# Optimization experiments

Measured on AMD Instinct MI355X. Metric: run time of the kernel, lower is better.

The kernel has to match this reference:

```python
import jax, jax.numpy as jnp
import numpy as np

N_NODES = 50000
N_EDGES = 600000
D_IN = 128
HID = 128
N_LAYERS = 4
N_OUT = 8
BN_EPS = 1e-5


def setup_inputs() -> dict:
    key = jax.random.key(0)
    ks = jax.random.split(key, 12)
    x = jax.random.normal(ks[0], (N_NODES, D_IN), dtype=jnp.float32)
    edge_index = jax.random.randint(ks[1], (2, N_EDGES), 0, N_NODES, dtype=jnp.int64)
    s = 1.0 / np.sqrt(HID)
    # per-layer GIN MLP params, stacked over layers (d_in == hidden so shapes match)
    W1 = jax.random.uniform(ks[2], (N_LAYERS, HID, HID), jnp.float32, -s, s)
    b1 = jax.random.uniform(ks[3], (N_LAYERS, HID), jnp.float32, -s, s)
    W2 = jax.random.uniform(ks[4], (N_LAYERS, HID, HID), jnp.float32, -s, s)
    b2 = jax.random.uniform(ks[5], (N_LAYERS, HID), jnp.float32, -s, s)
    gamma = jnp.ones((N_LAYERS, HID), jnp.float32)
    beta = jnp.zeros((N_LAYERS, HID), jnp.float32)
    s1 = 1.0 / np.sqrt(N_LAYERS * HID)
    lin1_W = jax.random.uniform(ks[6], (N_LAYERS * HID, HID), jnp.float32, -s1, s1)
    lin1_b = jax.random.uniform(ks[7], (HID,), jnp.float32, -s1, s1)
    lin2_W = jax.random.uniform(ks[8], (HID, N_OUT), jnp.float32, -s, s)
    lin2_b = jax.random.uniform(ks[9], (N_OUT,), jnp.float32, -s, s)
    return dict(x=x, edge_index=edge_index, W1=W1, b1=b1, W2=W2, b2=b2,
                gamma=gamma, beta=beta, lin1_W=lin1_W, lin1_b=lin1_b,
                lin2_W=lin2_W, lin2_b=lin2_b)


def _gin_layer(x, src, dst, W1, b1, W2, b2, g, bt):
    # GINConv, eps=0: h_i = MLP(x_i + sum_{j in N(i)} x_j)
    agg = jax.ops.segment_sum(x[src], dst, num_segments=N_NODES)  # [N, d]
    h = x + agg
    h = jax.nn.relu(h @ W1 + b1)
    h = jax.nn.relu(h @ W2 + b2)
    # BatchNorm1d (training-mode stats, biased variance)
    mean = jnp.mean(h, axis=0)
    var = jnp.var(h, axis=0)
    return (h - mean) * jax.lax.rsqrt(var + BN_EPS) * g + bt


def reference(x, edge_index, W1, b1, W2, b2, gamma, beta,
              lin1_W, lin1_b, lin2_W, lin2_b):
    src, dst = edge_index[0], edge_index[1]
    xs = []
    h = x
    for l in range(N_LAYERS):
        h = _gin_layer(h, src, dst, W1[l], b1[l], W2[l], b2[l], gamma[l], beta[l])
        xs.append(h)
    jk = jnp.concatenate(xs, axis=-1)          # JumpingKnowledge 'cat' -> [N, L*HID]
    out = jax.nn.relu(jk @ lin1_W + lin1_b)    # dropout is identity at inference
    out = out @ lin2_W + lin2_b                # [N, N_OUT]
    return out
```

## Files before the change

### kernel.cpp

```cpp
#include <hip/hip_runtime.h>

#define NNODES 50000
#define NEDGES 600000
#define HID 128
#define NLAYERS 4
#define NOUT 8
#define BN_EPS 1e-5f
#define NBLK 196
#define NPBLK 3125
#define NCOPY 8
#define IDXCAP 1024

typedef short short8 __attribute__((ext_vector_type(8)));
typedef float f32x4 __attribute__((ext_vector_type(4)));

__device__ inline unsigned short f2bf(float f) {
  unsigned u = __float_as_uint(f);
  unsigned r = ((u >> 16) & 1u) + 0x7fffu;
  return (unsigned short)((u + r) >> 16);
}
__device__ inline float bflo(unsigned w) { return __uint_as_float(w << 16); }
__device__ inline float bfhi(unsigned w) { return __uint_as_float(w & 0xffff0000u); }


__global__ void detect64_k(const int* __restrict__ ei, int* __restrict__ flag) {
  __shared__ int anynz;
  if (threadIdx.x == 0) anynz = 0;
  __syncthreads();
  int acc = 0;
  for (int i = threadIdx.x; i < 4096; i += 256) {
    int p = i * 146;
    acc |= ei[2 * p + 1];
  }
  if (acc != 0) anynz = 1;
  __syncthreads();
  if (threadIdx.x == 0) *flag = (anynz == 0) ? 1 : 0;
}

__global__ void cvt_bf_k(const float* __restrict__ src, unsigned short* __restrict__ dst,
                         int n4) {
  int i = blockIdx.x * 256 + threadIdx.x;
  if (i >= n4) return;
  float4 v = ((const float4*)src)[i];
  ushort4 o;
  o.x = f2bf(v.x);
  o.y = f2bf(v.y);
  o.z = f2bf(v.z);
  o.w = f2bf(v.w);
  ((ushort4*)dst)[i] = o;
}


__global__ void zero_degc_k(int* __restrict__ degC) {
  int i = blockIdx.x * 256 + threadIdx.x;
  if (i < NCOPY * NNODES) degC[i] = 0;
}

__global__ void hist_rank_k(const int* __restrict__ ei, const int* __restrict__ flag,
                            int* __restrict__ degC, int* __restrict__ rank) {
  int e = blockIdx.x * 256 + threadIdx.x;
  if (e >= NEDGES) return;
  int d = (*flag) ? ei[2 * NEDGES + 2 * e] : ei[NEDGES + e];
  int c = blockIdx.x & (NCOPY - 1);
  rank[e] = atomicAdd(&degC[c * NNODES + d], 1);
}

__global__ void coff_k(int* __restrict__ degC, int* __restrict__ deg) {
  int d = blockIdx.x * 256 + threadIdx.x;
  if (d >= NNODES) return;
  int run = 0;
#pragma unroll
  for (int c = 0; c < NCOPY; ++c) {
    int t = degC[c * NNODES + d];
    degC[c * NNODES + d] = run;
    run += t;
  }
  deg[d] = run;
}

__global__ void blocksum_k(const int* __restrict__ deg, int* __restrict__ bsum) {
  int t = threadIdx.x;
  int i = blockIdx.x * 256 + t;
  __shared__ int sh[256];
  sh[t] = (i < NNODES) ? deg[i] : 0;
  __syncthreads();
  for (int s = 128; s > 0; s >>= 1) {
    if (t < s) sh[t] += sh[t + s];
    __syncthreads();
  }
  if (t == 0) bsum[blockIdx.x] = sh[0];
}

__global__ void scanb_k(const int* __restrict__ bsum, int* __restrict__ boff) {
  __shared__ int sh[256];
  int t = threadIdx.x;
  sh[t] = (t < NBLK) ? bsum[t] : 0;
  __syncthreads();
  for (int d = 1; d < 256; d <<= 1) {
    int v = (t >= d) ? sh[t - d] : 0;
    __syncthreads();
    sh[t] += v;
    __syncthreads();
  }
  if (t < NBLK) boff[t] = (t == 0) ? 0 : sh[t - 1];
}

__global__ void writeoff_k(const int* __restrict__ deg, const int* __restrict__ boff,
                           int* __restrict__ off) {
  int t = threadIdx.x;
  int i = blockIdx.x * 256 + t;
  __shared__ int sh[256];
  int v = (i < NNODES) ? deg[i] : 0;
  sh[t] = v;
  __syncthreads();
  for (int d = 1; d < 256; d <<= 1) {
    int u = (t >= d) ? sh[t - d] : 0;
    __syncthreads();
    sh[t] += u;
    __syncthreads();
  }
  int excl = boff[blockIdx.x] + sh[t] - v;
  if (i < NNODES) off[i] = excl;
  if (i == NNODES - 1) off[NNODES] = excl + v;
}

__global__ void fill2_k(const int* __restrict__ ei, const int* __restrict__ flag,
                        const int* __restrict__ off, const int* __restrict__ degC,
                        const int* __restrict__ rank, int* __restrict__ srcs) {
  int e = blockIdx.x * 256 + threadIdx.x;
  if (e >= NEDGES) return;
  int s, d;
  if (*flag) {
    s = ei[2 * e];
    d = ei[2 * NEDGES + 2 * e];
  } else {
    s = ei[e];
    d = ei[NEDGES + e];
  }
  int c = blockIdx.x & (NCOPY - 1);
  srcs[off[d] + degC[c * NNODES + d] + rank[e]] = s;
}

template <bool AFFINE>
__global__ void gather_agg_k(const unsigned short* __restrict__ X,
                             const int* __restrict__ off, const int* __restrict__ srcs,
                             const float* __restrict__ ab, unsigned short* __restrict__ T) {
  __shared__ int sOff[9];
  __shared__ int sIdx[IDXCAP];
  int tid = threadIdx.x;
  int nb = blockIdx.x * 8;
  if (tid < 9) sOff[tid] = off[nb + tid];
  __syncthreads();
  int base = sOff[0];
  int total = sOff[8] - base;
  int stage = total > IDXCAP ? IDXCAP : total;
  for (int t = tid; t < stage; t += 256) sIdx[t] = srcs[base + t];
  __syncthreads();

  int g = tid >> 5, lane = tid & 31;
  int node = nb + g;
  int a = sOff[g] - base, bnd = sOff[g + 1] - base;
  const uint2* Xv = (const uint2*)X;
  uint2 w = Xv[(size_t)node * 32 + lane];
  float a0 = bflo(w.x), a1 = bfhi(w.x), a2 = bflo(w.y), a3 = bfhi(w.y);

  if (total <= IDXCAP) {
    int e = a;
#pragma unroll
    for (; e + 4 <= bnd; e += 4) {
      int s0 = sIdx[e], s1 = sIdx[e + 1], s2 = sIdx[e + 2], s3 = sIdx[e + 3];
      uint2 v0 = Xv[(size_t)s0 * 32 + lane];
      uint2 v1 = Xv[(size_t)s1 * 32 + lane];
      uint2 v2 = Xv[(size_t)s2 * 32 + lane];
      uint2 v3 = Xv[(size_t)s3 * 32 + lane];
      a0 += bflo(v0.x); a1 += bfhi(v0.x); a2 += bflo(v0.y); a3 += bfhi(v0.y);
      a0 += bflo(v1.x); a1 += bfhi(v1.x); a2 += bflo(v1.y); a3 += bfhi(v1.y);
      a0 += bflo(v2.x); a1 += bfhi(v2.x); a2 += bflo(v2.y); a3 += bfhi(v2.y);
      a0 += bflo(v3.x); a1 += bfhi(v3.x); a2 += bflo(v3.y); a3 += bfhi(v3.y);
    }
    for (; e < bnd; ++e) {
      int s = sIdx[e];
      uint2 v = Xv[(size_t)s * 32 + lane];
      a0 += bflo(v.x); a1 += bfhi(v.x); a2 += bflo(v.y); a3 += bfhi(v.y);
    }
  } else {
    for (int e = a; e < bnd; ++e) {
      int s = srcs[base + e];
      uint2 v = Xv[(size_t)s * 32 + lane];
      a0 += bflo(v.x); a1 += bfhi(v.x); a2 += bflo(v.y); a3 += bfhi(v.y);
    }
  }

  if (AFFINE) {
    float4 al = *(const float4*)(ab + lane * 4);
    float4 be = *(const float4*)(ab + 128 + lane * 4);
    float dp1 = (float)(bnd - a + 1);
    a0 = al.x * a0 + dp1 * be.x;
    a1 = al.y * a1 + dp1 * be.y;
    a2 = al.z * a2 + dp1 * be.z;
    a3 = al.w * a3 + dp1 * be.w;
  }

  uint2 o;
  o.x = (unsigned)f2bf(a0) | ((unsigned)f2bf(a1) << 16);
  o.y = (unsigned)f2bf(a2) | ((unsigned)f2bf(a3) << 16);
  ((uint2*)T)[(size_t)node * 32 + lane] = o;
}

__global__ void packW_k(const float* __restrict__ W1, const float* __restrict__ W2,
                        unsigned short* __restrict__ P) {
  int t = blockIdx.x * 256 + threadIdx.x;
  if (t >= 32 * 512) return;
  int gk = t >> 9;
  int nt = (t >> 6) & 7;
  int lane = t & 63;
  const float* src;
  int kbase;
  if (gk < 16) {
    src = W1 + (gk >> 2) * 16384;
    kbase = (gk & 3) * 32;
  } else {
    src = W2 + ((gk - 16) >> 2) * 16384;
    kbase = ((gk - 16) & 3) * 32;
  }
  int n = nt * 16 + (lane & 15);
  int k0 = kbase + (lane >> 4) * 8;
  unsigned short* dst = P + (size_t)t * 8;
#pragma unroll
  for (int j = 0; j < 8; ++j) dst[j] = f2bf(src[(size_t)(k0 + j) * HID + n]);
}

__global__ void packjk_k(const float* __restrict__ L1, const float* __restrict__ ab,
                         unsigned short* __restrict__ Pjk) {
  int t = blockIdx.x * 256 + threadIdx.x;
  if (t >= 16 * 512) return;
  int gk = t >> 9;
  int nt = (t >> 6) & 7;
  int lane = t & 63;
  int n = nt * 16 + (lane & 15);
  int k0 = gk * 32 + (lane >> 4) * 8;
  unsigned short* dst = Pjk + (size_t)t * 8;
#pragma unroll
  for (int j = 0; j < 8; ++j) {
    int K = k0 + j;
    float al = ab[(K >> 7) * 256 + (K & 127)];
    dst[j] = f2bf(al * L1[(size_t)K * HID + n]);
  }
}

__global__ void biasjk_k(const float* __restrict__ L1, const float* __restrict__ ab,
                         const float* __restrict__ l1b, float* __restrict__ bjk) {
  int n = threadIdx.x;
  float acc = l1b[n];
  for (int K = 0; K < 4 * HID; ++K) {
    float be = ab[(K >> 7) * 256 + 128 + (K & 127)];
    acc += be * L1[(size_t)K * HID + n];
  }
  bjk[n] = acc;
}

__global__ __launch_bounds__(128) void mlp_k(const unsigned short* __restrict__ A,
                                             const unsigned short* __restrict__ P1,
                                             const float* __restrict__ bias1,
                                             const unsigned short* __restrict__ P2,
                                             const float* __restrict__ bias2,
                                             unsigned short* __restrict__ Hq, int M,
                                             float* __restrict__ pstats) {
  __shared__ unsigned short sA[16 * 136];
  int tid = threadIdx.x;
  int lane = tid & 63, w = tid >> 6;
  int rb = blockIdx.x * 16;
  int r = rb + (lane & 15);
  int hi = lane >> 4, c = lane & 15;
  int koff = hi * 8;
  int ntb = w * 4;

  short8 a_[4];
  const unsigned short* Ar = A + (size_t)r * HID + koff;
#pragma unroll
  for (int ks = 0; ks < 4; ++ks) a_[ks] = *(const short8*)(Ar + ks * 32);

  const short8* Bp1 = (const short8*)P1;
  f32x4 acc[4];
#pragma unroll
  for (int nt = 0; nt < 4; ++nt) acc[nt] = (f32x4){0.f, 0.f, 0.f, 0.f};
  short8 bcur[4], bnxt[4];
#pragma unroll
  for (int nt = 0; nt < 4; ++nt) bcur[nt] = Bp1[(ntb + nt) * 64 + lane];
#pragma unroll
  for (int ks = 0; ks < 4; ++ks) {
    if (ks < 3) {
#pragma unroll
      for (int nt = 0; nt < 4; ++nt) bnxt[nt] = Bp1[(ks + 1) * 512 + (ntb + nt) * 64 + lane];
    }
#pragma unroll
    for (int nt = 0; nt < 4; ++nt)
      acc[nt] = __builtin_amdgcn_mfma_f32_16x16x32_bf16(a_[ks], bcur[nt], acc[nt], 0, 0, 0);
    if (ks < 3) {
#pragma unroll
      for (int nt = 0; nt < 4; ++nt) bcur[nt] = bnxt[nt];
    }
  }
#pragma unroll
  for (int nt = 0; nt < 4; ++nt) {
    int col = (ntb + nt) * 16 + c;
    float b = bias1[col];
#pragma unroll
    for (int rr = 0; rr < 4; ++rr) {
      float v = fmaxf(acc[nt][rr] + b, 0.f);
      sA[(hi * 4 + rr) * 136 + col] = f2bf(v);
    }
  }
  __syncthreads();

#pragma unroll
  for (int nt = 0; nt < 4; ++nt) acc[nt] = (f32x4){0.f, 0.f, 0.f, 0.f};
  const short8* Bp2 = (const short8*)P2;
#pragma unroll
  for (int nt = 0; nt < 4; ++nt) bcur[nt] = Bp2[(ntb + nt) * 64 + lane];
#pragma unroll
  for (int ks = 0; ks < 4; ++ks) {
    short8 af = *(const short8*)&sA[c * 136 + ks * 32 + koff];
    if (ks < 3) {
#pragma unroll
      for (int nt = 0; nt < 4; ++nt) bnxt[nt] = Bp2[(ks + 1) * 512 + (ntb + nt) * 64 + lane];
    }
#pragma unroll
    for (int nt = 0; nt < 4; ++nt)
      acc[nt] = __builtin_amdgcn_mfma_f32_16x16x32_bf16(af, bcur[nt], acc[nt], 0, 0, 0);
    if (ks < 3) {
#pragma unroll
      for (int nt = 0; nt < 4; ++nt) bcur[nt] = bnxt[nt];
    }
  }
  float* dst = pstats + (size_t)blockIdx.x * 256;
#pragma unroll
  for (int nt = 0; nt < 4; ++nt) {
    int col = (ntb + nt) * 16 + c;
    float b = bias2[col];
    float s = 0.f, q = 0.f;
#pragma unroll
    for (int rr = 0; rr < 4; ++rr) {
      int row = rb + hi * 4 + rr;
      float v = fmaxf(acc[nt][rr] + b, 0.f);
      Hq[(size_t)row * HID + col] = f2bf(v);
      s += v;
      q += v * v;
    }
    s += __shfl_xor(s, 16, 64);
    q += __shfl_xor(q, 16, 64);
    s += __shfl_xor(s, 32, 64);
    q += __shfl_xor(q, 32, 64);
    if (hi == 0) {
      dst[col] = s;
      dst[128 + col] = q;
    }
  }
}

__global__ void reduce_ab_k(const float* __restrict__ pstats, const float* __restrict__ gamma,
                            const float* __restrict__ beta, float* __restrict__ ab) {
  __shared__ float sh[256], sh2[256];
  int j = blockIdx.x;
  int t = threadIdx.x;
  float s = 0.f, q = 0.f;
  for (int b = t; b < NPBLK; b += 256) {
    s += pstats[(size_t)b * 256 + j];
    q += pstats[(size_t)b * 256 + 128 + j];
  }
  sh[t] = s;
  sh2[t] = q;
  __syncthreads();
  for (int st = 128; st > 0; st >>= 1) {
    if (t < st) {
      sh[t] += sh[t + st];
      sh2[t] += sh2[t + st];
    }
    __syncthreads();
  }
  if (t == 0) {
    const float invN = 1.0f / (float)NNODES;
    float m = sh[0] * invN;
    float var = sh2[0] * invN - m * m;
    float al = gamma[j] * rsqrtf(var + BN_EPS);
    ab[j] = al;
    ab[128 + j] = beta[j] - m * al;
  }
}

__global__ __launch_bounds__(128) void mjkgemm_k(const unsigned short* __restrict__ H0,
                                                 const unsigned short* __restrict__ H1,
                                                 const unsigned short* __restrict__ H2,
                                                 const unsigned short* __restrict__ H3,
                                                 const unsigned short* __restrict__ P,
                                                 const float* __restrict__ bias,
                                                 float* __restrict__ C, int M) {
  int tid = threadIdx.x;
  int lane = tid & 63, w = tid >> 6;
  int rb = blockIdx.x * 16;
  int r = rb + (lane & 15);
  int koff = (lane >> 4) * 8;
  int ntb = w * 4;
  f32x4 acc[4];
#pragma unroll
  for (int nt = 0; nt < 4; ++nt) acc[nt] = (f32x4){0.f, 0.f, 0.f, 0.f};
  const unsigned short* Hs[4] = {H0, H1, H2, H3};
  short8 bcur[4], bnxt[4];
  for (int l = 0; l < 4; ++l) {
    const short8* Bp = (const short8*)(P + l * 16384);
    short8 a_[4];
    const unsigned short* Ar = Hs[l] + (size_t)r * HID + koff;
#pragma unroll
    for (int ks = 0; ks < 4; ++ks) a_[ks] = *(const short8*)(Ar + ks * 32);
#pragma unroll
    for (int nt = 0; nt < 4; ++nt) bcur[nt] = Bp[(ntb + nt) * 64 + lane];
#pragma unroll
    for (int ks = 0; ks < 4; ++ks) {
      if (ks < 3) {
#pragma unroll
        for (int nt = 0; nt < 4; ++nt) bnxt[nt] = Bp[(ks + 1) * 512 + (ntb + nt) * 64 + lane];
      }
#pragma unroll
      for (int nt = 0; nt < 4; ++nt)
        acc[nt] = __builtin_amdgcn_mfma_f32_16x16x32_bf16(a_[ks], bcur[nt], acc[nt], 0, 0, 0);
      if (ks < 3) {
#pragma unroll
        for (int nt = 0; nt < 4; ++nt) bcur[nt] = bnxt[nt];
      }
    }
  }
  int hi = lane >> 4, c = lane & 15;
#pragma unroll
  for (int nt = 0; nt < 4; ++nt) {
    int col = (ntb + nt) * 16 + c;
    float b = bias[col];
#pragma unroll
    for (int rr = 0; rr < 4; ++rr) {
      int row = rb + hi * 4 + rr;
      float v = fmaxf(acc[nt][rr] + b, 0.f);
      C[(size_t)row * HID + col] = v;
    }
  }
}

__global__ void head_k(const float* __restrict__ O1, const float* __restrict__ W,
                       const float* __restrict__ b, float* __restrict__ out, int M) {
  __shared__ float sW[HID * NOUT];
  int tid = threadIdx.x;
#pragma unroll
  for (int i = 0; i < 4; ++i) sW[tid + i * 256] = W[tid + i * 256];
  __syncthreads();
  int row = blockIdx.x * 256 + tid;
  if (row >= M) return;
  float acc[NOUT];
#pragma unroll
  for (int j = 0; j < NOUT; ++j) acc[j] = b[j];
  const float* Ar = O1 + (size_t)row * HID;
  for (int k = 0; k < HID; k += 4) {
    float4 a = *(const float4*)(Ar + k);
#pragma unroll
    for (int kk = 0; kk < 4; ++kk) {
      float av = ((const float*)&a)[kk];
#pragma unroll
      for (int j = 0; j < NOUT; ++j) acc[j] += av * sW[(k + kk) * NOUT + j];
    }
  }
#pragma unroll
  for (int j = 0; j < NOUT; ++j) out[(size_t)row * NOUT + j] = acc[j];
}


extern "C" void kernel_launch(void* const* d_in, const int* in_sizes, int n_in,
                              void* d_out, int out_size, void* d_ws, size_t ws_size,
                              hipStream_t stream) {
  const float* x     = (const float*)d_in[0];
  const int*   ei    = (const int*)d_in[1];
  const float* W1    = (const float*)d_in[2];
  const float* b1    = (const float*)d_in[3];
  const float* W2    = (const float*)d_in[4];
  const float* b2    = (const float*)d_in[5];
  const float* gamma = (const float*)d_in[6];
  const float* beta  = (const float*)d_in[7];
  const float* l1W   = (const float*)d_in[8];
  const float* l1b   = (const float*)d_in[9];
  const float* l2W   = (const float*)d_in[10];
  const float* l2b   = (const float*)d_in[11];

  float* ws = (float*)d_ws;
  const size_t NB = (size_t)NNODES * HID;
  const size_t NBH = NB / 2;
  float* t2 = ws;
  unsigned short* xb = (unsigned short*)(ws + NB);
  unsigned short* tmp = (unsigned short*)(ws + NB + NBH);
  unsigned short* hq[4];
  for (int l = 0; l < 4; ++l)
    hq[l] = (unsigned short*)(ws + NB + (2 + l) * NBH);
  float* ab = ws + NB + 6 * NBH;
  float* bjk = ab + 1024;
  int* flag = (int*)(bjk + 128);
  int* deg = flag + 4;
  int* off = deg + (NNODES + 1);
  int* bsum = off + (NNODES + 1);
  int* boff = bsum + 256;
  int* degC = boff + 260;
  int* rank = degC + NCOPY * NNODES;
  int* srcs = rank + NEDGES;
  size_t pofs = NB + 6 * NBH + 1024 + 128 + 4 + 2 * (size_t)(NNODES + 1) + 256 + 260 +
                (size_t)NCOPY * NNODES + 2 * (size_t)NEDGES;
  pofs = (pofs + 3) & ~(size_t)3;
  unsigned short* P = (unsigned short*)(ws + pofs);
  unsigned short* Pjk = P + 131072;
  float* pstats = ws + pofs + 98304;

  detect64_k<<<1, 256, 0, stream>>>(ei, flag);
  zero_degc_k<<<1563, 256, 0, stream>>>(degC);
  hist_rank_k<<<2344, 256, 0, stream>>>(ei, flag, degC, rank);
  coff_k<<<NBLK, 256, 0, stream>>>(degC, deg);
  blocksum_k<<<NBLK, 256, 0, stream>>>(deg, bsum);
  scanb_k<<<1, 256, 0, stream>>>(bsum, boff);
  writeoff_k<<<NBLK, 256, 0, stream>>>(deg, boff, off);
  fill2_k<<<2344, 256, 0, stream>>>(ei, flag, off, degC, rank, srcs);
  packW_k<<<64, 256, 0, stream>>>(W1, W2, P);
  cvt_bf_k<<<6250, 256, 0, stream>>>(x, xb, NNODES * 32);

  for (int l = 0; l < NLAYERS; ++l) {
    if (l == 0)
      gather_agg_k<false><<<6250, 256, 0, stream>>>(xb, off, srcs, nullptr, tmp);
    else
      gather_agg_k<true><<<6250, 256, 0, stream>>>(hq[l - 1], off, srcs, ab + (l - 1) * 256,
                                                   tmp);
    mlp_k<<<NPBLK, 128, 0, stream>>>(tmp, P + (size_t)l * 16384, b1 + l * HID,
                                     P + 65536 + (size_t)l * 16384, b2 + l * HID, hq[l],
                                     NNODES, pstats);
    reduce_ab_k<<<128, 256, 0, stream>>>(pstats, gamma + l * HID, beta + l * HID,
                                         ab + l * 256);
  }
  packjk_k<<<32, 256, 0, stream>>>(l1W, ab, Pjk);
  biasjk_k<<<1, 128, 0, stream>>>(l1W, ab, l1b, bjk);
  mjkgemm_k<<<NPBLK, 128, 0, stream>>>(hq[0], hq[1], hq[2], hq[3], Pjk, bjk, t2, NNODES);
  head_k<<<196, 256, 0, stream>>>(t2, l2W, l2b, (float*)d_out, NNODES);
}
```

Baseline: 331.6 us.

## Fuse JK GEMM with output head and split BN stats reduction into two stages

```diff
diff --git a/kernel.cpp b/kernel.cpp
--- a/kernel.cpp
+++ b/kernel.cpp
@@ -10,6 +10,7 @@
 #define NPBLK 3125
 #define NCOPY 8
 #define IDXCAP 1024
+#define RED1 125
 
 typedef short short8 __attribute__((ext_vector_type(8)));
 typedef float f32x4 __attribute__((ext_vector_type(4)));
@@ -358,44 +359,49 @@
   }
 }
 
-__global__ void reduce_ab_k(const float* __restrict__ pstats, const float* __restrict__ gamma,
-                            const float* __restrict__ beta, float* __restrict__ ab) {
-  __shared__ float sh[256], sh2[256];
-  int j = blockIdx.x;
+__global__ void psum_k(const float* __restrict__ pstats, float* __restrict__ part) {
   int t = threadIdx.x;
-  float s = 0.f, q = 0.f;
-  for (int b = t; b < NPBLK; b += 256) {
-    s += pstats[(size_t)b * 256 + j];
-    q += pstats[(size_t)b * 256 + 128 + j];
-  }
-  sh[t] = s;
-  sh2[t] = q;
-  __syncthreads();
-  for (int st = 128; st > 0; st >>= 1) {
-    if (t < st) {
-      sh[t] += sh[t + st];
-      sh2[t] += sh2[t + st];
-    }
-    __syncthreads();
-  }
-  if (t == 0) {
+  size_t r0 = (size_t)blockIdx.x * 25;
+  float acc = 0.f;
+#pragma unroll 5
+  for (int r = 0; r < 25; ++r) acc += pstats[(r0 + r) * 256 + t];
+  part[(size_t)blockIdx.x * 256 + t] = acc;
+}
+
+__global__ void ab_k(const float* __restrict__ part, const float* __restrict__ gamma,
+                     const float* __restrict__ beta, float* __restrict__ ab) {
+  __shared__ float tot[256];
+  int t = threadIdx.x;
+  float acc = 0.f;
+  for (int k = 0; k < RED1; ++k) acc += part[(size_t)k * 256 + t];
+  tot[t] = acc;
+  __syncthreads();
+  if (t < 128) {
     const float invN = 1.0f / (float)NNODES;
-    float m = sh[0] * invN;
-    float var = sh2[0] * invN - m * m;
-    float al = gamma[j] * rsqrtf(var + BN_EPS);
-    ab[j] = al;
-    ab[128 + j] = beta[j] - m * al;
-  }
-}
-
-__global__ __launch_bounds__(128) void mjkgemm_k(const unsigned short* __restrict__ H0,
+    float m = tot[t] * invN;
+    float var = tot[128 + t] * invN - m * m;
+    float al = gamma[t] * rsqrtf(var + BN_EPS);
+    ab[t] = al;
+    ab[128 + t] = beta[t] - m * al;
+  }
+}
+
+__global__ __launch_bounds__(128) void mjkhead_k(const unsigned short* __restrict__ H0,
                                                  const unsigned short* __restrict__ H1,
                                                  const unsigned short* __restrict__ H2,
                                                  const unsigned short* __restrict__ H3,
                                                  const unsigned short* __restrict__ P,
                                                  const float* __restrict__ bias,
-                                                 float* __restrict__ C, int M) {
+                                                 const float* __restrict__ l2W,
+                                                 const float* __restrict__ l2b,
+                                                 float* __restrict__ out, int M) {
+  __shared__ float sT[16][136];
+  __shared__ float sW[HID * NOUT];
+  __shared__ float sb[NOUT];
   int tid = threadIdx.x;
+  for (int i = tid; i < HID * NOUT; i += 128) sW[i] = l2W[i];
+  if (tid < NOUT) sb[tid] = l2b[tid];
+
   int lane = tid & 63, w = tid >> 6;
   int rb = blockIdx.x * 16;
   int r = rb + (lane & 15);
@@ -436,37 +442,14 @@
     float b = bias[col];
 #pragma unroll
     for (int rr = 0; rr < 4; ++rr) {
-      int row = rb + hi * 4 + rr;
-      float v = fmaxf(acc[nt][rr] + b, 0.f);
-      C[(size_t)row * HID + col] = v;
-    }
-  }
-}
-
-__global__ void head_k(const float* __restrict__ O1, const float* __restrict__ W,
-                       const float* __restrict__ b, float* __restrict__ out, int M) {
-  __shared__ float sW[HID * NOUT];
-  int tid = threadIdx.x;
-#pragma unroll
-  for (int i = 0; i < 4; ++i) sW[tid + i * 256] = W[tid + i * 256];
-  __syncthreads();
-  int row = blockIdx.x * 256 + tid;
-  if (row >= M) return;
-  float acc[NOUT];
-#pragma unroll
-  for (int j = 0; j < NOUT; ++j) acc[j] = b[j];
-  const float* Ar = O1 + (size_t)row * HID;
-  for (int k = 0; k < HID; k += 4) {
-    float4 a = *(const float4*)(Ar + k);
-#pragma unroll
-    for (int kk = 0; kk < 4; ++kk) {
-      float av = ((const float*)&a)[kk];
-#pragma unroll
-      for (int j = 0; j < NOUT; ++j) acc[j] += av * sW[(k + kk) * NOUT + j];
-    }
-  }
-#pragma unroll
-  for (int j = 0; j < NOUT; ++j) out[(size_t)row * NOUT + j] = acc[j];
+      sT[hi * 4 + rr][col] = fmaxf(acc[nt][rr] + b, 0.f);
+    }
+  }
+  __syncthreads();
+  int row = tid >> 3, j = tid & 7;
+  float a = sb[j];
+  for (int k = 0; k < HID; ++k) a += sT[row][k] * sW[k * NOUT + j];
+  out[(size_t)(rb + row) * NOUT + j] = a;
 }
 
 
@@ -511,6 +494,7 @@
   unsigned short* P = (unsigned short*)(ws + pofs);
   unsigned short* Pjk = P + 131072;
   float* pstats = ws + pofs + 98304;
+  float* part = pstats + (size_t)NPBLK * 256;
 
   detect64_k<<<1, 256, 0, stream>>>(ei, flag);
   zero_degc_k<<<1563, 256, 0, stream>>>(degC);
@@ -532,11 +516,12 @@
     mlp_k<<<NPBLK, 128, 0, stream>>>(tmp, P + (size_t)l * 16384, b1 + l * HID,
                                      P + 65536 + (size_t)l * 16384, b2 + l * HID, hq[l],
                                      NNODES, pstats);
-    reduce_ab_k<<<128, 256, 0, stream>>>(pstats, gamma + l * HID, beta + l * HID,
-                                         ab + l * 256);
+    psum_k<<<RED1, 256, 0, stream>>>(pstats, part);
+    ab_k<<<1, 256, 0, stream>>>(part, gamma + l * HID, beta + l * HID, ab + l * 256);
   }
   packjk_k<<<32, 256, 0, stream>>>(l1W, ab, Pjk);
   biasjk_k<<<1, 128, 0, stream>>>(l1W, ab, l1b, bjk);
-  mjkgemm_k<<<NPBLK, 128, 0, stream>>>(hq[0], hq[1], hq[2], hq[3], Pjk, bjk, t2, NNODES);
-  head_k<<<196, 256, 0, stream>>>(t2, l2W, l2b, (float*)d_out, NNODES);
-}
+  mjkhead_k<<<NPBLK, 128, 0, stream>>>(hq[0], hq[1], hq[2], hq[3], Pjk, bjk, l2W, l2b,
+                                       (float*)d_out, NNODES);
+  (void)t2;
+}
```

Result: no change. 329.4 us (-0.7%).
